# Kernel tuning notes

Measured on AMD Instinct MI355X. Metric: run time of the kernel, lower is better.

## Reference

```python
import jax, jax.numpy as jnp
import numpy as np

BOARD = 361  # 19x19 Go board
SEQ = 24     # 8 history boards + 16 move boards


def setup_inputs() -> dict:
    key = jax.random.key(0)
    ks = jax.random.split(key, 12)
    B, H, L = 4096, 256, 2
    s = 1.0 / np.sqrt(H)  # PyTorch LSTM init scale
    u = lambda k, shape: jax.random.uniform(k, shape, jnp.float32, -s, s)
    return {
        "data": jax.random.randint(ks[0], (B, SEQ), 0, BOARD),
        "h0": jax.random.uniform(ks[1], (L * 2, B, H), jnp.float32),
        "c0": jax.random.uniform(ks[2], (L * 2, B, H), jnp.float32),
        "W_ih0": u(ks[3], (2, 4 * H, BOARD)),
        "W_hh0": u(ks[4], (2, 4 * H, H)),
        "b_ih0": u(ks[5], (2, 4 * H)),
        "b_hh0": u(ks[6], (2, 4 * H)),
        "W_ih1": u(ks[7], (2, 4 * H, 2 * H)),
        "W_hh1": u(ks[8], (2, 4 * H, H)),
        "b_ih1": u(ks[9], (2, 4 * H)),
        "b_hh1": u(ks[10], (2, 4 * H)),
    }


def _cell(x, h, c, Wih, Whh, bih, bhh):
    # PyTorch gate order: i, f, g, o
    g = x @ Wih.T + bih + h @ Whh.T + bhh
    i, f, gg, o = jnp.split(g, 4, axis=-1)
    c2 = jax.nn.sigmoid(f) * c + jax.nn.sigmoid(i) * jnp.tanh(gg)
    h2 = jax.nn.sigmoid(o) * jnp.tanh(c2)
    return h2, c2


def reference(data, h0, c0, W_ih0, W_hh0, b_ih0, b_hh0, W_ih1, W_hh1, b_ih1, b_hh1):
    # Fused one-hot construction: pos == -1 -> zero board (replaces nested scatter loops)
    onehot = jnp.where(
        data[..., None] >= 0,
        jax.nn.one_hot(jnp.maximum(data, 0), BOARD, dtype=jnp.float32),
        0.0,
    )  # [B, 24, 361]
    xs = jnp.swapaxes(onehot, 0, 1)  # [24, B, 361]
    layers = [(W_ih0, W_hh0, b_ih0, b_hh0), (W_ih1, W_hh1, b_ih1, b_hh1)]

    def step(carry, x):
        h, c = carry  # [L*2, B, H] each, index = layer*2 + direction
        new_h, new_c = [], []
        inp = x
        for l, (Wih, Whh, bih, bhh) in enumerate(layers):
            hs = []
            for d in range(2):
                idx = l * 2 + d
                h2, c2 = _cell(inp, h[idx], c[idx], Wih[d], Whh[d], bih[d], bhh[d])
                new_h.append(h2)
                new_c.append(c2)
                hs.append(h2)
            inp = jnp.concatenate(hs, axis=-1)  # [B, 2H] fed to next layer
        return (jnp.stack(new_h), jnp.stack(new_c)), inp

    _, ys = jax.lax.scan(step, (h0, c0), xs)  # ys: [24, B, 2H]
    return jnp.swapaxes(ys, 0, 1)  # [B, 24, 2H]
```

## Files before the change

### kernel.cpp

```cpp
#include <hip/hip_runtime.h>


typedef _Float16 f16x8 __attribute__((ext_vector_type(8)));
typedef float f32x4 __attribute__((ext_vector_type(4)));

#define NB 4096
#define SEQ 24
#define HB ((size_t)NB * 256)

__device__ __forceinline__ float bf2f(unsigned short u) {
  return __uint_as_float(((unsigned)u) << 16);
}
__device__ __forceinline__ unsigned short f2bf(float f) {
  unsigned x = __float_as_uint(f);
  x += 0x7fffu + ((x >> 16) & 1u);
  return (unsigned short)(x >> 16);
}
__device__ __forceinline__ float ldw(const void* p, size_t i, int isf32) {
  return isf32 ? ((const float*)p)[i] : bf2f(((const unsigned short*)p)[i]);
}
__device__ __forceinline__ float fsig(float x) {
  return __builtin_amdgcn_rcpf(1.f + __expf(-x));
}
__device__ __forceinline__ float ftanh(float x) {
  float ax = __builtin_fabsf(x);
  float z = __expf(-2.f * ax);
  float r = (1.f - z) * __builtin_amdgcn_rcpf(1.f + z);
  return __builtin_copysignf(r, x);
}
__device__ __forceinline__ void st_h(_Float16* p, float v) {
  unsigned short u = __builtin_bit_cast(unsigned short, (_Float16)v);
  __hip_atomic_store((unsigned short*)p, u, __ATOMIC_RELAXED,
                     __HIP_MEMORY_SCOPE_AGENT);
}

__global__ void k_sniff(const unsigned short* __restrict__ w, int* flag) {
  unsigned short u = w[threadIdx.x * 2];
  int e = (u >> 7) & 0xFF;
  if (e > 123) atomicOr(flag, 1);
}

__global__ void k_prep_wihT0b(const void* __restrict__ Wih0,
                              const void* __restrict__ bih0,
                              const void* __restrict__ bhh0,
                              const int* __restrict__ flag,
                              _Float16* __restrict__ outp) {
  const int isf32 = *flag;
  int idx = blockIdx.x * 256 + threadIdx.x;
  if (idx >= 2 * 362 * 1024) return;
  int n = idx & 1023;
  int p = (idx >> 10) % 362;
  int d = idx / (362 * 1024);
  float v = ldw(bih0, d * 1024 + n, isf32) + ldw(bhh0, d * 1024 + n, isf32);
  if (p < 361) v += ldw(Wih0, (size_t)(d * 1024 + n) * 361 + p, isf32);
  outp[idx] = (_Float16)v;
}

__global__ void k_prep_whh0(const void* __restrict__ Whh0,
                            const int* __restrict__ flag,
                            _Float16* __restrict__ outp) {
  const int isf32 = *flag;
  int idx = blockIdx.x * 256 + threadIdx.x;
  if (idx >= 2 * 1024 * 256) return;
  int jj = idx & 7, lane = (idx >> 3) & 63, kk = (idx >> 9) & 7;
  int nt = (idx >> 12) & 3, g = (idx >> 14) & 3, j = (idx >> 16) & 3, d = (idx >> 18) & 1;
  int row = g * 256 + j * 64 + nt * 16 + (lane & 15);
  int k = kk * 32 + (lane >> 4) * 8 + jj;
  outp[idx] = (_Float16)ldw(Whh0, (size_t)(d * 1024 + row) * 256 + k, isf32);
}

__global__ void k_prep_w1(const void* __restrict__ Wih1,
                          const void* __restrict__ Whh1,
                          const int* __restrict__ flag,
                          _Float16* __restrict__ outp) {
  const int isf32 = *flag;
  int idx = blockIdx.x * 256 + threadIdx.x;
  if (idx >= 2 * 1024 * 768) return;
  int jj = idx & 7, lane = (idx >> 3) & 63, kk = (idx >> 9) & 7;
  int rest = idx >> 12;
  int kc = rest % 3; rest /= 3;
  int nt = rest & 3; rest >>= 2;
  int g = rest & 3; rest >>= 2;
  int j = rest & 3; int d = rest >> 2;
  int row = g * 256 + j * 64 + nt * 16 + (lane & 15);
  int k = kc * 256 + kk * 32 + (lane >> 4) * 8 + jj;
  float v = (k < 512) ? ldw(Wih1, (size_t)(d * 1024 + row) * 512 + k, isf32)
                      : ldw(Whh1, (size_t)(d * 1024 + row) * 256 + (k - 512), isf32);
  outp[idx] = (_Float16)v;
}

__global__ void k_prep_bias1(const void* __restrict__ bih1,
                             const void* __restrict__ bhh1,
                             const int* __restrict__ flag,
                             float* __restrict__ outp) {
  const int isf32 = *flag;
  int idx = blockIdx.x * 256 + threadIdx.x;
  if (idx >= 2048) return;
  outp[idx] = ldw(bih1, idx, isf32) + ldw(bhh1, idx, isf32);
}

__global__ void k_prep_dataT(const int* __restrict__ data, int* __restrict__ dataT) {
  int idx = blockIdx.x * 256 + threadIdx.x;
  if (idx >= NB * SEQ) return;
  int row = idx / SEQ, t = idx % SEQ;
  dataT[t * NB + row] = data[idx];
}

__global__ void k_prep_h(const void* __restrict__ h0, const int* __restrict__ flag,
                         _Float16* __restrict__ h0buf, _Float16* __restrict__ h1buf) {
  const int isf32 = *flag;
  int idx = blockIdx.x * 256 + threadIdx.x;
  if (idx >= 4 * NB * 256) return;
  int ld = idx / (NB * 256);
  int r = idx % (NB * 256);
  _Float16 v = (_Float16)ldw(h0, (size_t)idx, isf32);
  if (ld < 2) h0buf[(size_t)(2 + ld) * HB + r] = v;
  else        h1buf[(size_t)ld * HB + r] = v;
}

__global__ __launch_bounds__(512, 2) void lstm_main(
    const int* __restrict__ dataT,
    const void* __restrict__ c0,
    const _Float16* __restrict__ wihT0b,
    const _Float16* __restrict__ whh0p,
    const _Float16* __restrict__ w1p,
    const float* __restrict__ bias1,
    const int* __restrict__ flag,
    unsigned* bar,
    _Float16* __restrict__ h0buf,
    _Float16* __restrict__ h1buf,
    void* __restrict__ out) {
  const int isf32 = *flag;
  const int tid = threadIdx.x;
  const int lane = tid & 63;
  const int wv = tid >> 6;
  const int n16 = lane & 15;
  const int q = lane >> 4;
  const int bid = blockIdx.x;
  const int rb = bid & 7;
  const int cgi = bid >> 3;
  const int d = cgi >> 4;
  const int hcb = cgi & 15;
  const int hc0 = hcb * 16;
  const int j4 = hcb >> 2, nt4 = hcb & 3;
  const int wrow = rb * 512 + wv * 64;

  extern __shared__ __align__(16) _Float16 lds[];
  _Float16* lw0 = lds;
  _Float16* lw1 = lds + 4 * 4096;

#pragma unroll
  for (int g = 0; g < 4; ++g) {
    const _Float16* s = whh0p + ((size_t)(((d * 4 + j4) * 4 + g) * 4 + nt4)) * 4096;
    *(f16x8*)&lw0[g * 4096 + tid * 8] = *(const f16x8*)&s[tid * 8];
  }
#pragma unroll
  for (int g = 0; g < 4; ++g)
#pragma unroll
    for (int kc = 0; kc < 3; ++kc) {
      const _Float16* s = w1p + ((size_t)((((d * 4 + j4) * 4 + g) * 4 + nt4) * 3 + kc)) * 4096;
      *(f16x8*)&lw1[(g * 3 + kc) * 4096 + tid * 8] = *(const f16x8*)&s[tid * 8];
    }

  float c0r[4][4], c1r[4][4];
#pragma unroll
  for (int mt = 0; mt < 4; ++mt)
#pragma unroll
    for (int rr = 0; rr < 4; ++rr) {
      int row = wrow + mt * 16 + q * 4 + rr;
      int col = hc0 + n16;
      c0r[mt][rr] = ldw(c0, ((size_t)d * NB + row) * 256 + col, isf32);
      c1r[mt][rr] = ldw(c0, ((size_t)(2 + d) * NB + row) * 256 + col, isf32);
    }
  float bvs[4];
#pragma unroll
  for (int g = 0; g < 4; ++g) bvs[g] = bias1[d * 1024 + g * 256 + hc0 + n16];
  __syncthreads();

  for (int p = 0; p <= SEQ; ++p) {
    if (p < SEQ) {
      const _Float16* hsrc = h0buf + ((size_t)(((p & 1) ^ 1) * 2 + d)) * HB;
      f16x8 a[4][8];
#pragma unroll
      for (int mt = 0; mt < 4; ++mt)
#pragma unroll
        for (int kk = 0; kk < 8; ++kk)
          a[mt][kk] = *(const f16x8*)&hsrc[(size_t)(wrow + mt * 16 + n16) * 256 + kk * 32 + q * 8];

      f32x4 acc[4][4];
#pragma unroll
      for (int mt = 0; mt < 4; ++mt) {
        int pos[4];
#pragma unroll
        for (int rr = 0; rr < 4; ++rr) {
          int v = dataT[p * NB + wrow + mt * 16 + q * 4 + rr];
          pos[rr] = (v < 0) ? 361 : v;
        }
#pragma unroll
        for (int g = 0; g < 4; ++g) {
          int col = g * 256 + hc0 + n16;
#pragma unroll
          for (int rr = 0; rr < 4; ++rr)
            acc[mt][g][rr] = (float)wihT0b[((size_t)(d * 362 + pos[rr])) * 1024 + col];
        }
      }
#pragma unroll
      for (int g = 0; g < 4; ++g) {
        f16x8 bf[8];
#pragma unroll
        for (int kk = 0; kk < 8; ++kk)
          bf[kk] = *(const f16x8*)&lw0[g * 4096 + kk * 512 + lane * 8];
#pragma unroll
        for (int mt = 0; mt < 4; ++mt)
#pragma unroll
          for (int kk = 0; kk < 8; ++kk)
            acc[mt][g] = __builtin_amdgcn_mfma_f32_16x16x32_f16(a[mt][kk], bf[kk], acc[mt][g], 0, 0, 0);
      }
      _Float16* hdst = h0buf + ((size_t)((p & 1) * 2 + d)) * HB;
#pragma unroll
      for (int mt = 0; mt < 4; ++mt)
#pragma unroll
        for (int rr = 0; rr < 4; ++rr) {
          float iv = fsig(acc[mt][0][rr]);
          float fv = fsig(acc[mt][1][rr]);
          float gv = ftanh(acc[mt][2][rr]);
          float ov = fsig(acc[mt][3][rr]);
          float cn = fv * c0r[mt][rr] + iv * gv;
          c0r[mt][rr] = cn;
          float hn = ov * ftanh(cn);
          st_h(&hdst[(size_t)(wrow + mt * 16 + q * 4 + rr) * 256 + hc0 + n16], hn);
        }
    }
    if (p >= 1) {
      const int t = p - 1;
      f32x4 acc[4][4];
#pragma unroll
      for (int mt = 0; mt < 4; ++mt)
#pragma unroll
        for (int g = 0; g < 4; ++g) {
          f32x4 b4 = {bvs[g], bvs[g], bvs[g], bvs[g]};
          acc[mt][g] = b4;
        }
#pragma unroll
      for (int kc = 0; kc < 3; ++kc) {
        const _Float16* base =
            (kc == 0) ? h0buf + ((size_t)((t & 1) * 2 + 0)) * HB
          : (kc == 1) ? h0buf + ((size_t)((t & 1) * 2 + 1)) * HB
                      : h1buf + ((size_t)(((t & 1) ^ 1) * 2 + d)) * HB;
        f16x8 a[4][8];
#pragma unroll
        for (int mt = 0; mt < 4; ++mt)
#pragma unroll
          for (int kk = 0; kk < 8; ++kk)
            a[mt][kk] = *(const f16x8*)&base[(size_t)(wrow + mt * 16 + n16) * 256 + kk * 32 + q * 8];
#pragma unroll
        for (int g = 0; g < 4; ++g) {
          f16x8 bf[8];
#pragma unroll
          for (int kk = 0; kk < 8; ++kk)
            bf[kk] = *(const f16x8*)&lw1[(g * 3 + kc) * 4096 + kk * 512 + lane * 8];
#pragma unroll
          for (int mt = 0; mt < 4; ++mt)
#pragma unroll
            for (int kk = 0; kk < 8; ++kk)
              acc[mt][g] = __builtin_amdgcn_mfma_f32_16x16x32_f16(a[mt][kk], bf[kk], acc[mt][g], 0, 0, 0);
        }
      }
      _Float16* hdst = h1buf + ((size_t)((t & 1) * 2 + d)) * HB;
#pragma unroll
      for (int mt = 0; mt < 4; ++mt)
#pragma unroll
        for (int rr = 0; rr < 4; ++rr) {
          float iv = fsig(acc[mt][0][rr]);
          float fv = fsig(acc[mt][1][rr]);
          float gv = ftanh(acc[mt][2][rr]);
          float ov = fsig(acc[mt][3][rr]);
          float cn = fv * c1r[mt][rr] + iv * gv;
          c1r[mt][rr] = cn;
          float hn = ov * ftanh(cn);
          int row = wrow + mt * 16 + q * 4 + rr;
          st_h(&hdst[(size_t)row * 256 + hc0 + n16], hn);
          size_t oi = ((size_t)row * SEQ + t) * 512 + d * 256 + hc0 + n16;
          if (isf32) __builtin_nontemporal_store(hn, &((float*)out)[oi]);
          else       __builtin_nontemporal_store(f2bf(hn), &((unsigned short*)out)[oi]);
        }
    }
    if (p < SEQ) {
      const unsigned tgt = 32u * (unsigned)(p + 1);
      unsigned* arr = bar + rb * 32;
      unsigned* rdy = bar + 256 + rb * 32;
      __syncthreads();
      if (tid == 0) {
        __hip_atomic_fetch_add(arr, 1u, __ATOMIC_RELAXED, __HIP_MEMORY_SCOPE_AGENT);
        while (__hip_atomic_load(arr, __ATOMIC_RELAXED, __HIP_MEMORY_SCOPE_AGENT) < tgt) {
          __builtin_amdgcn_s_sleep(1);
        }
      }
      __syncthreads();
      __builtin_amdgcn_fence(__ATOMIC_ACQUIRE, "agent");
      __syncthreads();
      if (tid == 0) {
        __hip_atomic_fetch_add(rdy, 1u, __ATOMIC_RELAXED, __HIP_MEMORY_SCOPE_AGENT);
        while (__hip_atomic_load(rdy, __ATOMIC_RELAXED, __HIP_MEMORY_SCOPE_AGENT) < tgt) {
          __builtin_amdgcn_s_sleep(1);
        }
      }
      __syncthreads();
    }
  }
}

extern "C" void kernel_launch(void* const* d_in, const int* in_sizes, int n_in,
                              void* d_out, int out_size, void* d_ws, size_t ws_size,
                              hipStream_t stream) {
  const int* data = (const int*)d_in[0];
  const void* h0 = d_in[1];
  const void* c0 = d_in[2];
  const void* Wih0 = d_in[3];
  const void* Whh0 = d_in[4];
  const void* bih0 = d_in[5];
  const void* bhh0 = d_in[6];
  const void* Wih1 = d_in[7];
  const void* Whh1 = d_in[8];
  const void* bih1 = d_in[9];
  const void* bhh1 = d_in[10];

  char* ws = (char*)d_ws;
  _Float16* wihT0b = (_Float16*)ws;
  _Float16* whh0p = (_Float16*)(ws + 1482752);
  _Float16* w1p   = (_Float16*)(ws + 2531328);
  float* b1       = (float*)(ws + 5677056);
  int* flag       = (int*)(ws + 5685248);
  unsigned* bar   = (unsigned*)(ws + 5685504);
  int* dataT      = (int*)(ws + 5687552);
  _Float16* h0buf = (_Float16*)(ws + 6080768);
  _Float16* h1buf = (_Float16*)(ws + 14469376);

  hipMemsetAsync(flag, 0, 256 + 2048, stream);
  k_sniff<<<1, 256, 0, stream>>>((const unsigned short*)Wih0, flag);
  k_prep_wihT0b<<<(2 * 362 * 1024 + 255) / 256, 256, 0, stream>>>(Wih0, bih0, bhh0, flag, wihT0b);
  k_prep_whh0<<<(2 * 1024 * 256 + 255) / 256, 256, 0, stream>>>(Whh0, flag, whh0p);
  k_prep_w1<<<(2 * 1024 * 768 + 255) / 256, 256, 0, stream>>>(Wih1, Whh1, flag, w1p);
  k_prep_bias1<<<8, 256, 0, stream>>>(bih1, bhh1, flag, b1);
  k_prep_dataT<<<(NB * SEQ + 255) / 256, 256, 0, stream>>>(data, dataT);
  k_prep_h<<<(4 * NB * 256 + 255) / 256, 256, 0, stream>>>(h0, flag, h0buf, h1buf);

  (void)hipFuncSetAttribute((const void*)lstm_main,
                            hipFuncAttributeMaxDynamicSharedMemorySize, 131072);

  const int* a0 = dataT;
  const void* a1 = c0;
  const _Float16* a2 = wihT0b;
  const _Float16* a3 = whh0p;
  const _Float16* a4 = w1p;
  const float* a5 = b1;
  const int* a6 = flag;
  unsigned* a7 = bar;
  _Float16* a8 = h0buf;
  _Float16* a9 = h1buf;
  void* a10 = d_out;
  void* kargs[] = {&a0, &a1, &a2, &a3, &a4, &a5, &a6, &a7, &a8, &a9, &a10};
  hipLaunchCooperativeKernel((const void*)lstm_main, dim3(256), dim3(512),
                             kargs, 131072, stream);
}
```

Baseline: 2.065 ms.

## Collapse two-phase grid barrier into single counter and detect same-XCD groups

At startup each block reads its XCC id and records it in a per-row-group mask, so the code can tell whether all 32 blocks of a row group sit on one XCD. If they do, h state is written with plain stores and the acquire fence is skipped, relying on the shared L2. In every case the per-step barrier drops from two arrive/wait phases to one counter. The risk is a memory-ordering hazard: plain stores and relaxed atomics without release semantics may leave stale h visible to other blocks, and the single-counter barrier could let a fast block overwrite the double buffer early.

```diff
diff --git a/kernel.cpp b/kernel.cpp
--- a/kernel.cpp
+++ b/kernel.cpp
@@ -148,6 +148,7 @@
   extern __shared__ __align__(16) _Float16 lds[];
   _Float16* lw0 = lds;
   _Float16* lw1 = lds + 4 * 4096;
+  __shared__ int fast_s;
 
 #pragma unroll
   for (int g = 0; g < 4; ++g) {
@@ -175,7 +176,22 @@
   float bvs[4];
 #pragma unroll
   for (int g = 0; g < 4; ++g) bvs[g] = bias1[d * 1024 + g * 256 + hc0 + n16];
+
+  unsigned xcc = __builtin_amdgcn_s_getreg(6164);
+  if (tid == 0) {
+    unsigned* pre = bar + rb * 32 + 8;
+    unsigned* msk = bar + rb * 32 + 16;
+    __hip_atomic_fetch_or(msk, 1u << (xcc & 31u), __ATOMIC_RELAXED,
+                          __HIP_MEMORY_SCOPE_AGENT);
+    asm volatile("s_waitcnt vmcnt(0)" ::: "memory");
+    __hip_atomic_fetch_add(pre, 1u, __ATOMIC_RELAXED, __HIP_MEMORY_SCOPE_AGENT);
+    while (__hip_atomic_load(pre, __ATOMIC_RELAXED, __HIP_MEMORY_SCOPE_AGENT) < 32u)
+      __builtin_amdgcn_s_sleep(1);
+    unsigned m = __hip_atomic_load(msk, __ATOMIC_RELAXED, __HIP_MEMORY_SCOPE_AGENT);
+    fast_s = ((m & (m - 1u)) == 0u) ? 1 : 0;
+  }
   __syncthreads();
+  const bool fast = (fast_s != 0);
 
   for (int p = 0; p <= SEQ; ++p) {
     if (p < SEQ) {
@@ -217,6 +233,7 @@
             acc[mt][g] = __builtin_amdgcn_mfma_f32_16x16x32_f16(a[mt][kk], bf[kk], acc[mt][g], 0, 0, 0);
       }
       _Float16* hdst = h0buf + ((size_t)((p & 1) * 2 + d)) * HB;
+      float hnv[4][4];
 #pragma unroll
       for (int mt = 0; mt < 4; ++mt)
 #pragma unroll
@@ -227,9 +244,23 @@
           float ov = fsig(acc[mt][3][rr]);
           float cn = fv * c0r[mt][rr] + iv * gv;
           c0r[mt][rr] = cn;
-          float hn = ov * ftanh(cn);
-          st_h(&hdst[(size_t)(wrow + mt * 16 + q * 4 + rr) * 256 + hc0 + n16], hn);
-        }
+          hnv[mt][rr] = ov * ftanh(cn);
+        }
+      if (fast) {
+#pragma unroll
+        for (int mt = 0; mt < 4; ++mt)
+#pragma unroll
+          for (int rr = 0; rr < 4; ++rr)
+            hdst[(size_t)(wrow + mt * 16 + q * 4 + rr) * 256 + hc0 + n16] =
+                (_Float16)hnv[mt][rr];
+      } else {
+#pragma unroll
+        for (int mt = 0; mt < 4; ++mt)
+#pragma unroll
+          for (int rr = 0; rr < 4; ++rr)
+            st_h(&hdst[(size_t)(wrow + mt * 16 + q * 4 + rr) * 256 + hc0 + n16],
+                 hnv[mt][rr]);
+      }
     }
     if (p >= 1) {
       const int t = p - 1;
@@ -267,6 +298,7 @@
         }
       }
       _Float16* hdst = h1buf + ((size_t)((t & 1) * 2 + d)) * HB;
+      float hnv[4][4];
 #pragma unroll
       for (int mt = 0; mt < 4; ++mt)
 #pragma unroll
@@ -278,34 +310,40 @@
           float cn = fv * c1r[mt][rr] + iv * gv;
           c1r[mt][rr] = cn;
           float hn = ov * ftanh(cn);
+          hnv[mt][rr] = hn;
           int row = wrow + mt * 16 + q * 4 + rr;
-          st_h(&hdst[(size_t)row * 256 + hc0 + n16], hn);
           size_t oi = ((size_t)row * SEQ + t) * 512 + d * 256 + hc0 + n16;
           if (isf32) __builtin_nontemporal_store(hn, &((float*)out)[oi]);
           else       __builtin_nontemporal_store(f2bf(hn), &((unsigned short*)out)[oi]);
         }
+      if (fast) {
+#pragma unroll
+        for (int mt = 0; mt < 4; ++mt)
+#pragma unroll
+          for (int rr = 0; rr < 4; ++rr)
+            hdst[(size_t)(wrow + mt * 16 + q * 4 + rr) * 256 + hc0 + n16] =
+                (_Float16)hnv[mt][rr];
+      } else {
+#pragma unroll
+        for (int mt = 0; mt < 4; ++mt)
+#pragma unroll
+          for (int rr = 0; rr < 4; ++rr)
+            st_h(&hdst[(size_t)(wrow + mt * 16 + q * 4 + rr) * 256 + hc0 + n16],
+                 hnv[mt][rr]);
+      }
     }
     if (p < SEQ) {
-      const unsigned tgt = 32u * (unsigned)(p + 1);
-      unsigned* arr = bar + rb * 32;
-      unsigned* rdy = bar + 256 + rb * 32;
       __syncthreads();
       if (tid == 0) {
-        __hip_atomic_fetch_add(arr, 1u, __ATOMIC_RELAXED, __HIP_MEMORY_SCOPE_AGENT);
-        while (__hip_atomic_load(arr, __ATOMIC_RELAXED, __HIP_MEMORY_SCOPE_AGENT) < tgt) {
+        unsigned* ctr = bar + rb * 32;
+        __hip_atomic_fetch_add(ctr, 1u, __ATOMIC_RELAXED, __HIP_MEMORY_SCOPE_AGENT);
+        const unsigned tgt = 32u * (unsigned)(p + 1);
+        while (__hip_atomic_load(ctr, __ATOMIC_RELAXED, __HIP_MEMORY_SCOPE_AGENT) < tgt) {
           __builtin_amdgcn_s_sleep(1);
         }
       }
       __syncthreads();
-      __builtin_amdgcn_fence(__ATOMIC_ACQUIRE, "agent");
-      __syncthreads();
-      if (tid == 0) {
-        __hip_atomic_fetch_add(rdy, 1u, __ATOMIC_RELAXED, __HIP_MEMORY_SCOPE_AGENT);
-        while (__hip_atomic_load(rdy, __ATOMIC_RELAXED, __HIP_MEMORY_SCOPE_AGENT) < tgt) {
-          __builtin_amdgcn_s_sleep(1);
-        }
-      }
-      __syncthreads();
+      if (!fast) __builtin_amdgcn_fence(__ATOMIC_ACQUIRE, "agent");
     }
   }
 }
```

Result: faster. 1.678 ms (-18.7%).
